# Optimization experiments

Measured on AMD Instinct MI355X. Metric: run time of the kernel, lower is better.

Reference implementation:

```python
import jax, jax.numpy as jnp
import numpy as np

LEAKY_SLOPE = 0.2  # PyG GATConv default negative_slope
EPS = 1e-16


def _gat_layer(h_in, src, dst, W, a_src, a_dst, b, concat):
    # h_in: [N, Fin]; src/dst: [Etot] (self-loops included); W: [Fin, H*C]
    N = h_in.shape[0]
    H, C = a_src.shape
    h = (h_in @ W).reshape(N, H, C)                       # [N,H,C]
    al_s = jnp.sum(h * a_src, axis=-1)                    # [N,H]
    al_d = jnp.sum(h * a_dst, axis=-1)                    # [N,H]
    e = jax.nn.leaky_relu(al_s[src] + al_d[dst], LEAKY_SLOPE)  # [E,H]
    emax = jax.ops.segment_max(e, dst, num_segments=N)    # segment softmax over dst
    p = jnp.exp(e - emax[dst])
    denom = jax.ops.segment_sum(p, dst, num_segments=N)
    alpha = p / (denom[dst] + EPS)                        # [E,H]
    out = jax.ops.segment_sum(h[src] * alpha[:, :, None], dst, num_segments=N)  # [N,H,C]
    out = out.reshape(N, H * C) if concat else out.mean(axis=1)
    return out + b


def setup_inputs() -> dict:
    key = jax.random.key(0)
    ks = jax.random.split(key, 16)
    N, E, Fin, Hd, Hh = 10000, 320000, 256, 128, 4

    def glorot(k, shape, fan_in):
        return jax.random.normal(k, shape, dtype=jnp.float32) * (1.0 / np.sqrt(fan_in))

    inp = {
        "x": jax.random.normal(ks[0], (N, Fin), dtype=jnp.float32),
        "edge_index": jax.random.randint(ks[1], (2, E), 0, N, dtype=jnp.int32),
        # conv1: Fin -> Hd x Hh heads, concat
        "W1": glorot(ks[2], (Fin, Hh * Hd), Fin),
        "a1_src": glorot(ks[3], (Hh, Hd), Hd),
        "a1_dst": glorot(ks[4], (Hh, Hd), Hd),
        "b1": jnp.zeros((Hh * Hd,), jnp.float32),
        # conv2: Hh*Hd -> Hd x Hh heads, concat
        "W2": glorot(ks[5], (Hh * Hd, Hh * Hd), Hh * Hd),
        "a2_src": glorot(ks[6], (Hh, Hd), Hd),
        "a2_dst": glorot(ks[7], (Hh, Hd), Hd),
        "b2": jnp.zeros((Hh * Hd,), jnp.float32),
        # conv3: Hh*Hd -> Hd, 1 head, concat=False (mean)
        "W3": glorot(ks[8], (Hh * Hd, Hd), Hh * Hd),
        "a3_src": glorot(ks[9], (1, Hd), Hd),
        "a3_dst": glorot(ks[10], (1, Hd), Hd),
        "b3": jnp.zeros((Hd,), jnp.float32),
        # classifier: Hd -> Hd//2 -> 2
        "Wc1": glorot(ks[11], (Hd, Hd // 2), Hd),
        "bc1": jnp.zeros((Hd // 2,), jnp.float32),
        "Wc2": glorot(ks[12], (Hd // 2, 2), Hd // 2),
        "bc2": jnp.zeros((2,), jnp.float32),
    }
    return inp


def reference(x, edge_index, W1, a1_src, a1_dst, b1, W2, a2_src, a2_dst, b2,
              W3, a3_src, a3_dst, b3, Wc1, bc1, Wc2, bc2):
    N = x.shape[0]
    loops = jnp.arange(N, dtype=edge_index.dtype)
    src = jnp.concatenate([edge_index[0], loops])  # PyG adds self-loops
    dst = jnp.concatenate([edge_index[1], loops])

    h = jax.nn.elu(_gat_layer(x, src, dst, W1, a1_src, a1_dst, b1, concat=True))
    h = jax.nn.elu(_gat_layer(h, src, dst, W2, a2_src, a2_dst, b2, concat=True))
    embeddings = _gat_layer(h, src, dst, W3, a3_src, a3_dst, b3, concat=False)  # [N, 128]
    out = jax.nn.relu(embeddings @ Wc1 + bc1) @ Wc2 + bc2  # [N, 2]
    return out, embeddings
```

## Files before the change

kernel.cpp:

```cpp
#include <hip/hip_runtime.h>
#include <cstddef>

#define LEAKY 0.2f
#define EPS_DEN 1e-16f

typedef short bf8_t __attribute__((ext_vector_type(8)));
typedef float f4_t __attribute__((ext_vector_type(4)));
typedef unsigned short us4_t __attribute__((ext_vector_type(4)));

__device__ __forceinline__ unsigned short f2bf(float f) {
    unsigned u = __float_as_uint(f);
    unsigned r = (u + 0x7fffu + ((u >> 16) & 1u)) >> 16;
    return (unsigned short)r;
}
__device__ __forceinline__ float bf2f(unsigned short h) {
    return __uint_as_float(((unsigned)h) << 16);
}

__global__ void hist_kernel(const int* __restrict__ dst, int* __restrict__ counts, int E) {
    int i = blockIdx.x * blockDim.x + threadIdx.x;
    if (i < E) atomicAdd(&counts[dst[i]], 1);
}

__global__ void scan1_kernel(int* __restrict__ cnt, int* __restrict__ bsum, int N) {
    __shared__ int s[256];
    int t = threadIdx.x;
    int i = blockIdx.x * 256 + t;
    int v = (i < N) ? cnt[i] : 0;
    s[t] = v;
    __syncthreads();
#pragma unroll
    for (int st = 1; st < 256; st <<= 1) {
        int add = (t >= st) ? s[t - st] : 0;
        __syncthreads();
        s[t] += add;
        __syncthreads();
    }
    if (i < N) cnt[i] = s[t] - v;
    if (t == 255) bsum[blockIdx.x] = s[255];
}

__global__ void scan2_kernel(int* __restrict__ bsum, int* __restrict__ offs, int NB, int N) {
    int t = threadIdx.x;
    int v = (t < NB) ? bsum[t] : 0;
    int inc = v;
#pragma unroll
    for (int off = 1; off < 64; off <<= 1) {
        int u = __shfl_up(inc, off);
        if (t >= off) inc += u;
    }
    if (t < NB) bsum[t] = inc - v;
    if (t == 63) offs[N] = inc;
}

__global__ void scan3_kernel(int* __restrict__ cnt, const int* __restrict__ bsum,
                             int* __restrict__ offs, int N) {
    int i = blockIdx.x * 256 + threadIdx.x;
    if (i < N) {
        int o = cnt[i] + bsum[blockIdx.x];
        offs[i] = o;
        cnt[i] = o;
    }
}

__global__ void scatter_kernel(const int* __restrict__ src, const int* __restrict__ dst,
                               int* __restrict__ cursor, int* __restrict__ csrc, int E) {
    int i = blockIdx.x * blockDim.x + threadIdx.x;
    if (i < E) {
        int d = dst[i];
        int pos = atomicAdd(&cursor[d], 1);
        csrc[pos] = src[i];
    }
}

__global__ void split_kernel(const float* __restrict__ in, unsigned short* __restrict__ hi,
                             unsigned short* __restrict__ lo, int len) {
    int i = blockIdx.x * blockDim.x + threadIdx.x;
    if (i >= len) return;
    float v = in[i];
    unsigned short h = f2bf(v);
    hi[i] = h;
    lo[i] = f2bf(v - bf2f(h));
}

__global__ void wsplit_kernel(const float* __restrict__ W, unsigned short* __restrict__ hi,
                              unsigned short* __restrict__ lo, int K, int N) {
    int idx = blockIdx.x * blockDim.x + threadIdx.x;
    if (idx >= K * N) return;
    int n = idx / K, k = idx % K;
    float v = W[(size_t)k * N + n];
    unsigned short h = f2bf(v);
    hi[idx] = h;
    lo[idx] = f2bf(v - bf2f(h));
}

__global__ __launch_bounds__(256) void mfma_gemm128_kernel(
    const unsigned short* __restrict__ Ahi, const unsigned short* __restrict__ Alo,
    const unsigned short* __restrict__ BThi, const unsigned short* __restrict__ BTlo,
    float* __restrict__ C, int M, int N, int K) {
    constexpr int BK = 32;
    __shared__ __align__(16) unsigned short sA[128 * BK];
    __shared__ __align__(16) unsigned short sB[128 * BK];
    int t = threadIdx.x;
    int w = t >> 6, lane = t & 63;
    int quad = lane >> 4, low = lane & 15;
    int m0 = blockIdx.y * 128, n0 = blockIdx.x * 128;
    int wm = (w & 1) * 64, wn = (w >> 1) * 64;

    f4_t acc[4][4];
#pragma unroll
    for (int i = 0; i < 4; i++)
#pragma unroll
        for (int j = 0; j < 4; j++) acc[i][j] = (f4_t){0.f, 0.f, 0.f, 0.f};

    int srow = lane >> 2;
    int schunk = lane & 3;

    const unsigned short* Ap[3] = {Ahi, Ahi, Alo};
    const unsigned short* Bp[3] = {BThi, BTlo, BThi};

    for (int pass = 0; pass < 3; pass++) {
        const unsigned short* A = Ap[pass];
        const unsigned short* B = Bp[pass];
        for (int k0 = 0; k0 < K; k0 += BK) {
            __syncthreads();
#pragma unroll
            for (int inst = 0; inst < 2; inst++) {
                int r = w * 32 + inst * 16 + srow;
                int gm = m0 + r;
                if (gm >= M) gm = M - 1;
                const void* g = (const void*)(A + (size_t)gm * K + k0 + schunk * 8);
                void* l = (void*)((char*)sA + (size_t)(w * 2048 + inst * 1024));
                __builtin_amdgcn_global_load_lds((const __attribute__((address_space(1))) void*)g,
                                                 (__attribute__((address_space(3))) void*)l, 16, 0, 0);
            }
#pragma unroll
            for (int inst = 0; inst < 2; inst++) {
                int r = w * 32 + inst * 16 + srow;
                int gn = n0 + r;
                const void* g = (const void*)(B + (size_t)gn * K + k0 + schunk * 8);
                void* l = (void*)((char*)sB + (size_t)(w * 2048 + inst * 1024));
                __builtin_amdgcn_global_load_lds((const __attribute__((address_space(1))) void*)g,
                                                 (__attribute__((address_space(3))) void*)l, 16, 0, 0);
            }
            __syncthreads();

            bf8_t af[4], bf[4];
#pragma unroll
            for (int i = 0; i < 4; i++) {
                int row = wm + i * 16 + low;
                af[i] = *(const bf8_t*)&sA[row * BK + quad * 8];
            }
#pragma unroll
            for (int j = 0; j < 4; j++) {
                int row = wn + j * 16 + low;
                bf[j] = *(const bf8_t*)&sB[row * BK + quad * 8];
            }
#pragma unroll
            for (int i = 0; i < 4; i++)
#pragma unroll
                for (int j = 0; j < 4; j++)
                    acc[i][j] = __builtin_amdgcn_mfma_f32_16x16x32_bf16(af[i], bf[j], acc[i][j], 0, 0, 0);
        }
    }

#pragma unroll
    for (int i = 0; i < 4; i++) {
#pragma unroll
        for (int r = 0; r < 4; r++) {
            int gm = m0 + wm + i * 16 + quad * 4 + r;
            if (gm >= M) continue;
#pragma unroll
            for (int j = 0; j < 4; j++) {
                int gn = n0 + wn + j * 16 + low;
                C[(size_t)gm * N + gn] = acc[i][j][r];
            }
        }
    }
}

__global__ __launch_bounds__(256) void mfma_gemm64_kernel(
    const unsigned short* __restrict__ Ahi, const unsigned short* __restrict__ Alo,
    const unsigned short* __restrict__ BThi, const unsigned short* __restrict__ BTlo,
    float* __restrict__ C, int M, int N, int K) {
    constexpr int BK = 32;
    __shared__ __align__(16) unsigned short sA[64 * BK];
    __shared__ __align__(16) unsigned short sB[128 * BK];
    int t = threadIdx.x;
    int w = t >> 6, lane = t & 63;
    int quad = lane >> 4, low = lane & 15;
    int m0 = blockIdx.y * 64, n0 = blockIdx.x * 128;
    int wm = (w & 1) * 32, wn = (w >> 1) * 64;

    f4_t acc[2][4];
#pragma unroll
    for (int i = 0; i < 2; i++)
#pragma unroll
        for (int j = 0; j < 4; j++) acc[i][j] = (f4_t){0.f, 0.f, 0.f, 0.f};

    int srow = lane >> 2;
    int schunk = lane & 3;

    const unsigned short* Ap[3] = {Ahi, Ahi, Alo};
    const unsigned short* Bp[3] = {BThi, BTlo, BThi};

    for (int pass = 0; pass < 3; pass++) {
        const unsigned short* A = Ap[pass];
        const unsigned short* B = Bp[pass];
        for (int k0 = 0; k0 < K; k0 += BK) {
            __syncthreads();
            {
                int gm = m0 + w * 16 + srow;
                if (gm >= M) gm = M - 1;
                const void* g = (const void*)(A + (size_t)gm * K + k0 + schunk * 8);
                void* l = (void*)((char*)sA + (size_t)(w * 1024));
                __builtin_amdgcn_global_load_lds((const __attribute__((address_space(1))) void*)g,
                                                 (__attribute__((address_space(3))) void*)l, 16, 0, 0);
            }
#pragma unroll
            for (int inst = 0; inst < 2; inst++) {
                int gn = n0 + w * 32 + inst * 16 + srow;
                const void* g = (const void*)(B + (size_t)gn * K + k0 + schunk * 8);
                void* l = (void*)((char*)sB + (size_t)(w * 2048 + inst * 1024));
                __builtin_amdgcn_global_load_lds((const __attribute__((address_space(1))) void*)g,
                                                 (__attribute__((address_space(3))) void*)l, 16, 0, 0);
            }
            __syncthreads();

            bf8_t af[2], bf[4];
#pragma unroll
            for (int i = 0; i < 2; i++) {
                int row = wm + i * 16 + low;
                af[i] = *(const bf8_t*)&sA[row * BK + quad * 8];
            }
#pragma unroll
            for (int j = 0; j < 4; j++) {
                int row = wn + j * 16 + low;
                bf[j] = *(const bf8_t*)&sB[row * BK + quad * 8];
            }
#pragma unroll
            for (int i = 0; i < 2; i++)
#pragma unroll
                for (int j = 0; j < 4; j++)
                    acc[i][j] = __builtin_amdgcn_mfma_f32_16x16x32_bf16(af[i], bf[j], acc[i][j], 0, 0, 0);
        }
    }

#pragma unroll
    for (int i = 0; i < 2; i++) {
#pragma unroll
        for (int r = 0; r < 4; r++) {
            int gm = m0 + wm + i * 16 + quad * 4 + r;
            if (gm >= M) continue;
#pragma unroll
            for (int j = 0; j < 4; j++) {
                int gn = n0 + wn + j * 16 + low;
                C[(size_t)gm * N + gn] = acc[i][j][r];
            }
        }
    }
}

__global__ void al_h4_kernel(const float* __restrict__ h, const float* __restrict__ a_src,
                             const float* __restrict__ a_dst, float* __restrict__ als,
                             float* __restrict__ ald, int N) {
    int wave = threadIdx.x >> 6, lane = threadIdx.x & 63;
    int n = blockIdx.x * 4 + wave;
    if (n >= N) return;
    const float* row = h + (size_t)n * 512;
    float ps[4] = {0, 0, 0, 0}, pd[4] = {0, 0, 0, 0};
#pragma unroll
    for (int k = 0; k < 8; k++) {
        int f = k * 64 + lane;
        float v = row[f];
        ps[k >> 1] += v * a_src[f];
        pd[k >> 1] += v * a_dst[f];
    }
#pragma unroll
    for (int off = 32; off; off >>= 1) {
#pragma unroll
        for (int hd = 0; hd < 4; hd++) {
            ps[hd] += __shfl_down(ps[hd], off);
            pd[hd] += __shfl_down(pd[hd], off);
        }
    }
    if (lane == 0) {
#pragma unroll
        for (int hd = 0; hd < 4; hd++) {
            als[n * 4 + hd] = ps[hd];
            ald[n * 4 + hd] = pd[hd];
        }
    }
}

__global__ void al_h1_kernel(const float* __restrict__ h, const float* __restrict__ a_src,
                             const float* __restrict__ a_dst, float* __restrict__ als,
                             float* __restrict__ ald, int N) {
    int wave = threadIdx.x >> 6, lane = threadIdx.x & 63;
    int n = blockIdx.x * 4 + wave;
    if (n >= N) return;
    const float* row = h + (size_t)n * 128;
    float v0 = row[lane], v1 = row[lane + 64];
    float ps = v0 * a_src[lane] + v1 * a_src[lane + 64];
    float pd = v0 * a_dst[lane] + v1 * a_dst[lane + 64];
#pragma unroll
    for (int off = 32; off; off >>= 1) {
        ps += __shfl_down(ps, off);
        pd += __shfl_down(pd, off);
    }
    if (lane == 0) { als[n] = ps; ald[n] = pd; }
}

__global__ void stats_h4_kernel(const int* __restrict__ csrc, const int* __restrict__ offs,
                                const float* __restrict__ als, const float* __restrict__ ald,
                                float* __restrict__ pbuf, float* __restrict__ psf,
                                float* __restrict__ rden, int N, int E) {
    int wave = threadIdx.x >> 6, lane = threadIdx.x & 63;
    int n = blockIdx.x * 4 + wave;
    if (n >= N) return;
    int hd = lane & 3, es = lane >> 2;
    float aldn = ald[n * 4 + hd];
    float selfe = als[n * 4 + hd] + aldn;
    selfe = selfe > 0.f ? selfe : LEAKY * selfe;
    int beg = offs[n], end = offs[n + 1];
    float* pb = pbuf + (size_t)hd * E;
    float m = selfe;
    for (int base = beg; base + es < end; base += 16) {
        int idx = base + es;
        int s = csrc[idx];
        float e = als[s * 4 + hd] + aldn;
        e = e > 0.f ? e : LEAKY * e;
        pb[idx] = e;
        m = fmaxf(m, e);
    }
#pragma unroll
    for (int off = 4; off < 64; off <<= 1) m = fmaxf(m, __shfl_xor(m, off));
    float d = 0.f;
    for (int base = beg; base + es < end; base += 16) {
        int idx = base + es;
        float p = __expf(pb[idx] - m);
        pb[idx] = p;
        d += p;
    }
#pragma unroll
    for (int off = 4; off < 64; off <<= 1) d += __shfl_xor(d, off);
    float pself = __expf(selfe - m);
    float r = 1.0f / (d + pself + EPS_DEN);
    if (es == 0) {
        psf[n * 4 + hd] = pself;
        rden[n * 4 + hd] = r;
    }
}

__global__ void stats_h1_kernel(const int* __restrict__ csrc, const int* __restrict__ offs,
                                const float* __restrict__ als, const float* __restrict__ ald,
                                float* __restrict__ pbuf, float* __restrict__ psf,
                                float* __restrict__ rden, int N) {
    int wave = threadIdx.x >> 6, lane = threadIdx.x & 63;
    int n = blockIdx.x * 4 + wave;
    if (n >= N) return;
    float aldn = ald[n];
    float selfe = als[n] + aldn;
    selfe = selfe > 0.f ? selfe : LEAKY * selfe;
    int beg = offs[n], end = offs[n + 1];
    float m = selfe;
    for (int base = beg; base + lane < end; base += 64) {
        int idx = base + lane;
        int s = csrc[idx];
        float e = als[s] + aldn;
        e = e > 0.f ? e : LEAKY * e;
        pbuf[idx] = e;
        m = fmaxf(m, e);
    }
#pragma unroll
    for (int off = 1; off < 64; off <<= 1) m = fmaxf(m, __shfl_xor(m, off));
    float d = 0.f;
    for (int base = beg; base + lane < end; base += 64) {
        int idx = base + lane;
        float p = __expf(pbuf[idx] - m);
        pbuf[idx] = p;
        d += p;
    }
#pragma unroll
    for (int off = 1; off < 64; off <<= 1) d += __shfl_xor(d, off);
    float pself = __expf(selfe - m);
    float r = 1.0f / (d + pself + EPS_DEN);
    if (lane == 0) { psf[n] = pself; rden[n] = r; }
}

template <bool DO_ELU>
__global__ __launch_bounds__(64) void gat_agg_hh_kernel(
    const float* __restrict__ h, const float* __restrict__ pbuf,
    const float* __restrict__ psf, const float* __restrict__ rden,
    const int* __restrict__ csrc, const int* __restrict__ offs,
    const float* __restrict__ bias, unsigned short* __restrict__ ohi,
    unsigned short* __restrict__ olo, int N, int E) {
    int gid = blockIdx.x;
    int hh = gid & 7;
    int n = gid >> 3;
    int head = hh >> 1;
    int lane = threadIdx.x;
    int eg = lane >> 4;
    int f0 = hh * 64 + (lane & 15) * 4;
    const float* pb = pbuf + (size_t)head * E;

    f4_t acc = (f4_t){0.f, 0.f, 0.f, 0.f};
    __shared__ int sSrc[64];
    __shared__ float sP[64];
    int beg = offs[n], end = offs[n + 1];
    for (int base = beg; base < end; base += 64) {
        int len = min(64, end - base);
        __syncthreads();
        if (lane < len) {
            sSrc[lane] = csrc[base + lane];
            sP[lane] = pb[base + lane];
        }
        __syncthreads();
#pragma unroll 8
        for (int c = eg; c < len; c += 4) {
            const float* srow = h + (size_t)sSrc[c] * 512;
            f4_t x = *(const f4_t*)(srow + f0);
            acc += sP[c] * x;
        }
    }
    if (eg == 0) {
        f4_t x = *(const f4_t*)(h + (size_t)n * 512 + f0);
        acc += psf[n * 4 + head] * x;
    }
#pragma unroll
    for (int j = 0; j < 4; j++) {
        acc[j] += __shfl_xor(acc[j], 16);
        acc[j] += __shfl_xor(acc[j], 32);
    }
    if (lane < 16) {
        float r = rden[n * 4 + head];
        f4_t b = *(const f4_t*)(bias + f0);
        us4_t hs, ls;
#pragma unroll
        for (int j = 0; j < 4; j++) {
            float o = acc[j] * r + b[j];
            if (DO_ELU) o = o > 0.f ? o : (__expf(o) - 1.0f);
            unsigned short hhh = f2bf(o);
            hs[j] = hhh;
            ls[j] = f2bf(o - bf2f(hhh));
        }
        size_t idx = (size_t)n * 512 + f0;
        *(us4_t*)&ohi[idx] = hs;
        *(us4_t*)&olo[idx] = ls;
    }
}

__global__ __launch_bounds__(64) void gat_agg_h1_cls_kernel(
    const float* __restrict__ h, const float* __restrict__ pbuf,
    const float* __restrict__ psf, const float* __restrict__ rden,
    const int* __restrict__ csrc, const int* __restrict__ offs,
    const float* __restrict__ bias, const float* __restrict__ Wc1,
    const float* __restrict__ bc1, const float* __restrict__ Wc2,
    const float* __restrict__ bc2, float* __restrict__ emb,
    float* __restrict__ outp, int N) {
    int n = blockIdx.x;
    int lane = threadIdx.x;
    int half = lane >> 5;
    int f0 = (lane & 31) * 4;

    f4_t acc = (f4_t){0.f, 0.f, 0.f, 0.f};
    __shared__ int sSrc[64];
    __shared__ float sP[64];
    __shared__ float semb[128];
    int beg = offs[n], end = offs[n + 1];
    for (int base = beg; base < end; base += 64) {
        int len = min(64, end - base);
        __syncthreads();
        if (lane < len) {
            sSrc[lane] = csrc[base + lane];
            sP[lane] = pbuf[base + lane];
        }
        __syncthreads();
#pragma unroll 8
        for (int c = half; c < len; c += 2) {
            const float* srow = h + (size_t)sSrc[c] * 128;
            f4_t x = *(const f4_t*)(srow + f0);
            acc += sP[c] * x;
        }
    }
    if (half == 0) {
        f4_t x = *(const f4_t*)(h + (size_t)n * 128 + f0);
        acc += psf[n] * x;
    }
#pragma unroll
    for (int j = 0; j < 4; j++) acc[j] += __shfl_xor(acc[j], 32);

    __syncthreads();
    if (half == 0) {
        float r = rden[n];
        f4_t b = *(const f4_t*)(bias + f0);
        f4_t o;
#pragma unroll
        for (int j = 0; j < 4; j++) o[j] = acc[j] * r + b[j];
        *(f4_t*)&semb[f0] = o;
        *(f4_t*)&emb[(size_t)n * 128 + f0] = o;
    }
    __syncthreads();

    float cacc = bc1[lane];
#pragma unroll 4
    for (int k = 0; k < 128; k++) cacc += semb[k] * Wc1[k * 64 + lane];
    cacc = fmaxf(cacc, 0.f);
    float o0 = cacc * Wc2[lane * 2 + 0];
    float o1 = cacc * Wc2[lane * 2 + 1];
#pragma unroll
    for (int off = 32; off; off >>= 1) {
        o0 += __shfl_down(o0, off);
        o1 += __shfl_down(o1, off);
    }
    if (lane == 0) {
        outp[n * 2 + 0] = o0 + bc2[0];
        outp[n * 2 + 1] = o1 + bc2[1];
    }
}

extern "C" void kernel_launch(void* const* d_in, const int* in_sizes, int n_in,
                              void* d_out, int out_size, void* d_ws, size_t ws_size,
                              hipStream_t stream) {
    const float* x      = (const float*)d_in[0];
    const int*   ei     = (const int*)d_in[1];
    const float* W1     = (const float*)d_in[2];
    const float* a1s    = (const float*)d_in[3];
    const float* a1d    = (const float*)d_in[4];
    const float* b1     = (const float*)d_in[5];
    const float* W2     = (const float*)d_in[6];
    const float* a2s    = (const float*)d_in[7];
    const float* a2d    = (const float*)d_in[8];
    const float* b2     = (const float*)d_in[9];
    const float* W3     = (const float*)d_in[10];
    const float* a3s    = (const float*)d_in[11];
    const float* a3d    = (const float*)d_in[12];
    const float* b3     = (const float*)d_in[13];
    const float* Wc1    = (const float*)d_in[14];
    const float* bc1    = (const float*)d_in[15];
    const float* Wc2    = (const float*)d_in[16];
    const float* bc2    = (const float*)d_in[17];

    const int N = in_sizes[0] / 256;
    const int E = in_sizes[1] / 2;
    const int F = 512;

    const int* src = ei;
    const int* dst = ei + E;

    auto align = [](size_t o) { return (o + 255) & ~(size_t)255; };
    size_t o = 0;
    size_t o_G     = o; o = align(o + (size_t)N * F * 4);
    size_t o_ahi   = o; o = align(o + (size_t)N * F * 2);
    size_t o_alo   = o; o = align(o + (size_t)N * F * 2);
    size_t o_xhi   = o; o = align(o + (size_t)N * 256 * 2);
    size_t o_xlo   = o; o = align(o + (size_t)N * 256 * 2);
    size_t o_w1h   = o; o = align(o + (size_t)512 * 256 * 2);
    size_t o_w1l   = o; o = align(o + (size_t)512 * 256 * 2);
    size_t o_w2h   = o; o = align(o + (size_t)512 * 512 * 2);
    size_t o_w2l   = o; o = align(o + (size_t)512 * 512 * 2);
    size_t o_w3h   = o; o = align(o + (size_t)128 * 512 * 2);
    size_t o_w3l   = o; o = align(o + (size_t)128 * 512 * 2);
    size_t o_als   = o; o = align(o + (size_t)N * 4 * 4);
    size_t o_ald   = o; o = align(o + (size_t)N * 4 * 4);
    size_t o_psf   = o; o = align(o + (size_t)N * 4 * 4);
    size_t o_rden  = o; o = align(o + (size_t)N * 4 * 4);
    size_t o_cnt   = o; o = align(o + (size_t)N * 4);
    size_t o_off   = o; o = align(o + (size_t)(N + 1) * 4);
    size_t o_bsum  = o; o = align(o + (size_t)64 * 4);
    size_t o_csrc  = o; o = align(o + (size_t)E * 4);
    size_t o_ebuf  = o; o = align(o + (size_t)E * 4 * 4);
    (void)ws_size;

    char* ws = (char*)d_ws;
    float* bufG  = (float*)(ws + o_G);
    unsigned short* act_hi = (unsigned short*)(ws + o_ahi);
    unsigned short* act_lo = (unsigned short*)(ws + o_alo);
    unsigned short* x_hi   = (unsigned short*)(ws + o_xhi);
    unsigned short* x_lo   = (unsigned short*)(ws + o_xlo);
    unsigned short* w1h = (unsigned short*)(ws + o_w1h);
    unsigned short* w1l = (unsigned short*)(ws + o_w1l);
    unsigned short* w2h = (unsigned short*)(ws + o_w2h);
    unsigned short* w2l = (unsigned short*)(ws + o_w2l);
    unsigned short* w3h = (unsigned short*)(ws + o_w3h);
    unsigned short* w3l = (unsigned short*)(ws + o_w3l);
    float* als  = (float*)(ws + o_als);
    float* ald  = (float*)(ws + o_ald);
    float* psf  = (float*)(ws + o_psf);
    float* rden = (float*)(ws + o_rden);
    int*   cnt  = (int*)(ws + o_cnt);
    int*   offs = (int*)(ws + o_off);
    int*   bsum = (int*)(ws + o_bsum);
    int*   csrc = (int*)(ws + o_csrc);
    float* ebuf = (float*)(ws + o_ebuf);

    float* outp = (float*)d_out;
    float* emb  = (float*)d_out + (size_t)N * 2;

    hipMemsetAsync(cnt, 0, (size_t)N * 4, stream);
    int eb = (E + 255) / 256;
    int nbs = (N + 255) / 256;
    hipLaunchKernelGGL(hist_kernel, dim3(eb), dim3(256), 0, stream, dst, cnt, E);
    hipLaunchKernelGGL(scan1_kernel, dim3(nbs), dim3(256), 0, stream, cnt, bsum, N);
    hipLaunchKernelGGL(scan2_kernel, dim3(1), dim3(64), 0, stream, bsum, offs, nbs, N);
    hipLaunchKernelGGL(scan3_kernel, dim3(nbs), dim3(256), 0, stream, cnt, bsum, offs, N);
    hipLaunchKernelGGL(scatter_kernel, dim3(eb), dim3(256), 0, stream, src, dst, cnt, csrc, E);

    hipLaunchKernelGGL(split_kernel, dim3((N * 256 + 255) / 256), dim3(256), 0, stream,
                       x, x_hi, x_lo, N * 256);
    hipLaunchKernelGGL(wsplit_kernel, dim3((256 * 512 + 255) / 256), dim3(256), 0, stream,
                       W1, w1h, w1l, 256, 512);
    hipLaunchKernelGGL(wsplit_kernel, dim3((512 * 512 + 255) / 256), dim3(256), 0, stream,
                       W2, w2h, w2l, 512, 512);
    hipLaunchKernelGGL(wsplit_kernel, dim3((512 * 128 + 255) / 256), dim3(256), 0, stream,
                       W3, w3h, w3l, 512, 128);

    int nb4 = (N + 3) / 4;
    int gy128 = (N + 127) / 128;
    int gy64  = (N + 63) / 64;

    hipLaunchKernelGGL(mfma_gemm128_kernel, dim3(512 / 128, gy128), dim3(256), 0, stream,
                       x_hi, x_lo, w1h, w1l, bufG, N, 512, 256);
    hipLaunchKernelGGL(al_h4_kernel, dim3(nb4), dim3(256), 0, stream, bufG, a1s, a1d, als, ald, N);
    hipLaunchKernelGGL(stats_h4_kernel, dim3(nb4), dim3(256), 0, stream,
                       csrc, offs, als, ald, ebuf, psf, rden, N, E);
    hipLaunchKernelGGL((gat_agg_hh_kernel<true>), dim3(N * 8), dim3(64), 0, stream,
                       bufG, ebuf, psf, rden, csrc, offs, b1, act_hi, act_lo, N, E);

    hipLaunchKernelGGL(mfma_gemm128_kernel, dim3(512 / 128, gy128), dim3(256), 0, stream,
                       act_hi, act_lo, w2h, w2l, bufG, N, 512, 512);
    hipLaunchKernelGGL(al_h4_kernel, dim3(nb4), dim3(256), 0, stream, bufG, a2s, a2d, als, ald, N);
    hipLaunchKernelGGL(stats_h4_kernel, dim3(nb4), dim3(256), 0, stream,
                       csrc, offs, als, ald, ebuf, psf, rden, N, E);
    hipLaunchKernelGGL((gat_agg_hh_kernel<true>), dim3(N * 8), dim3(64), 0, stream,
                       bufG, ebuf, psf, rden, csrc, offs, b2, act_hi, act_lo, N, E);

    hipLaunchKernelGGL(mfma_gemm64_kernel, dim3(128 / 128, gy64), dim3(256), 0, stream,
                       act_hi, act_lo, w3h, w3l, bufG, N, 128, 512);
    hipLaunchKernelGGL(al_h1_kernel, dim3(nb4), dim3(256), 0, stream, bufG, a3s, a3d, als, ald, N);
    hipLaunchKernelGGL(stats_h1_kernel, dim3(nb4), dim3(256), 0, stream,
                       csrc, offs, als, ald, ebuf, psf, rden, N);
    hipLaunchKernelGGL(gat_agg_h1_cls_kernel, dim3(N), dim3(64), 0, stream,
                       bufG, ebuf, psf, rden, csrc, offs, b3, Wc1, bc1, Wc2, bc2, emb, outp, N);
}
```

Measured before the change: 391.7 us.

## Fuse split-bf16 GEMM passes into one K loop and drop LDS staging in aggregation

The two split-precision bf16 MFMA GEMMs used to make three separate passes over K, reloading tiles each time. They now load the hi and lo tiles of A and B together per K step and reuse the hi fragments across all three MFMA products. This cuts global-to-LDS traffic and barrier count, at the cost of double the LDS footprint per block. The aggregation kernels also stop staging edge indices and weights through shared memory with barriers. Each lane now reads its edges directly, covering 8 features with more edge groups in flight.

Result: faster. 383.5 us (-2.1%).

```diff
diff --git a/kernel.cpp b/kernel.cpp
--- a/kernel.cpp
+++ b/kernel.cpp
@@ -7,6 +7,7 @@
 typedef short bf8_t __attribute__((ext_vector_type(8)));
 typedef float f4_t __attribute__((ext_vector_type(4)));
 typedef unsigned short us4_t __attribute__((ext_vector_type(4)));
+typedef unsigned short us8_t __attribute__((ext_vector_type(8)));
 
 __device__ __forceinline__ unsigned short f2bf(float f) {
     unsigned u = __float_as_uint(f);
@@ -99,8 +100,10 @@
     const unsigned short* __restrict__ BThi, const unsigned short* __restrict__ BTlo,
     float* __restrict__ C, int M, int N, int K) {
     constexpr int BK = 32;
-    __shared__ __align__(16) unsigned short sA[128 * BK];
-    __shared__ __align__(16) unsigned short sB[128 * BK];
+    __shared__ __align__(16) unsigned short sAh[128 * BK];
+    __shared__ __align__(16) unsigned short sAl[128 * BK];
+    __shared__ __align__(16) unsigned short sBh[128 * BK];
+    __shared__ __align__(16) unsigned short sBl[128 * BK];
     int t = threadIdx.x;
     int w = t >> 6, lane = t & 63;
     int quad = lane >> 4, low = lane & 15;
@@ -116,52 +119,73 @@
     int srow = lane >> 2;
     int schunk = lane & 3;
 
-    const unsigned short* Ap[3] = {Ahi, Ahi, Alo};
-    const unsigned short* Bp[3] = {BThi, BTlo, BThi};
-
-    for (int pass = 0; pass < 3; pass++) {
-        const unsigned short* A = Ap[pass];
-        const unsigned short* B = Bp[pass];
-        for (int k0 = 0; k0 < K; k0 += BK) {
-            __syncthreads();
-#pragma unroll
-            for (int inst = 0; inst < 2; inst++) {
-                int r = w * 32 + inst * 16 + srow;
-                int gm = m0 + r;
-                if (gm >= M) gm = M - 1;
-                const void* g = (const void*)(A + (size_t)gm * K + k0 + schunk * 8);
-                void* l = (void*)((char*)sA + (size_t)(w * 2048 + inst * 1024));
-                __builtin_amdgcn_global_load_lds((const __attribute__((address_space(1))) void*)g,
-                                                 (__attribute__((address_space(3))) void*)l, 16, 0, 0);
-            }
-#pragma unroll
-            for (int inst = 0; inst < 2; inst++) {
-                int r = w * 32 + inst * 16 + srow;
-                int gn = n0 + r;
-                const void* g = (const void*)(B + (size_t)gn * K + k0 + schunk * 8);
-                void* l = (void*)((char*)sB + (size_t)(w * 2048 + inst * 1024));
-                __builtin_amdgcn_global_load_lds((const __attribute__((address_space(1))) void*)g,
-                                                 (__attribute__((address_space(3))) void*)l, 16, 0, 0);
-            }
-            __syncthreads();
-
-            bf8_t af[4], bf[4];
-#pragma unroll
-            for (int i = 0; i < 4; i++) {
-                int row = wm + i * 16 + low;
-                af[i] = *(const bf8_t*)&sA[row * BK + quad * 8];
-            }
-#pragma unroll
-            for (int j = 0; j < 4; j++) {
-                int row = wn + j * 16 + low;
-                bf[j] = *(const bf8_t*)&sB[row * BK + quad * 8];
-            }
-#pragma unroll
-            for (int i = 0; i < 4; i++)
-#pragma unroll
-                for (int j = 0; j < 4; j++)
-                    acc[i][j] = __builtin_amdgcn_mfma_f32_16x16x32_bf16(af[i], bf[j], acc[i][j], 0, 0, 0);
-        }
+    for (int k0 = 0; k0 < K; k0 += BK) {
+        __syncthreads();
+#pragma unroll
+        for (int inst = 0; inst < 2; inst++) {
+            int r = w * 32 + inst * 16 + srow;
+            int gm = m0 + r;
+            if (gm >= M) gm = M - 1;
+            size_t goff = (size_t)gm * K + k0 + schunk * 8;
+            size_t loff = (size_t)(w * 2048 + inst * 1024);
+            __builtin_amdgcn_global_load_lds(
+                (const __attribute__((address_space(1))) void*)(Ahi + goff),
+                (__attribute__((address_space(3))) void*)((char*)sAh + loff), 16, 0, 0);
+            __builtin_amdgcn_global_load_lds(
+                (const __attribute__((address_space(1))) void*)(Alo + goff),
+                (__attribute__((address_space(3))) void*)((char*)sAl + loff), 16, 0, 0);
+        }
+#pragma unroll
+        for (int inst = 0; inst < 2; inst++) {
+            int r = w * 32 + inst * 16 + srow;
+            int gn = n0 + r;
+            size_t goff = (size_t)gn * K + k0 + schunk * 8;
+            size_t loff = (size_t)(w * 2048 + inst * 1024);
+            __builtin_amdgcn_global_load_lds(
+                (const __attribute__((address_space(1))) void*)(BThi + goff),
+                (__attribute__((address_space(3))) void*)((char*)sBh + loff), 16, 0, 0);
+            __builtin_amdgcn_global_load_lds(
+                (const __attribute__((address_space(1))) void*)(BTlo + goff),
+                (__attribute__((address_space(3))) void*)((char*)sBl + loff), 16, 0, 0);
+        }
+        __syncthreads();
+
+        bf8_t afh[4], bfh[4], x[4];
+#pragma unroll
+        for (int i = 0; i < 4; i++) {
+            int row = wm + i * 16 + low;
+            afh[i] = *(const bf8_t*)&sAh[row * BK + quad * 8];
+        }
+#pragma unroll
+        for (int j = 0; j < 4; j++) {
+            int row = wn + j * 16 + low;
+            bfh[j] = *(const bf8_t*)&sBh[row * BK + quad * 8];
+        }
+#pragma unroll
+        for (int i = 0; i < 4; i++)
+#pragma unroll
+            for (int j = 0; j < 4; j++)
+                acc[i][j] = __builtin_amdgcn_mfma_f32_16x16x32_bf16(afh[i], bfh[j], acc[i][j], 0, 0, 0);
+#pragma unroll
+        for (int j = 0; j < 4; j++) {
+            int row = wn + j * 16 + low;
+            x[j] = *(const bf8_t*)&sBl[row * BK + quad * 8];
+        }
+#pragma unroll
+        for (int i = 0; i < 4; i++)
+#pragma unroll
+            for (int j = 0; j < 4; j++)
+                acc[i][j] = __builtin_amdgcn_mfma_f32_16x16x32_bf16(afh[i], x[j], acc[i][j], 0, 0, 0);
+#pragma unroll
+        for (int i = 0; i < 4; i++) {
+            int row = wm + i * 16 + low;
+            x[i] = *(const bf8_t*)&sAl[row * BK + quad * 8];
+        }
+#pragma unroll
+        for (int i = 0; i < 4; i++)
+#pragma unroll
+            for (int j = 0; j < 4; j++)
+                acc[i][j] = __builtin_amdgcn_mfma_f32_16x16x32_bf16(x[i], bfh[j], acc[i][j], 0, 0, 0);
     }
 
 #pragma unroll
@@ -184,8 +208,10 @@
     const unsigned short* __restrict__ BThi, const unsigned short* __restrict__ BTlo,
     float* __restrict__ C, int M, int N, int K) {
     constexpr int BK = 32;
-    __shared__ __align__(16) unsigned short sA[64 * BK];
-    __shared__ __align__(16) unsigned short sB[128 * BK];
+    __shared__ __align__(16) unsigned short sAh[64 * BK];
+    __shared__ __align__(16) unsigned short sAl[64 * BK];
+    __shared__ __align__(16) unsigned short sBh[128 * BK];
+    __shared__ __align__(16) unsigned short sBl[128 * BK];
     int t = threadIdx.x;
     int w = t >> 6, lane = t & 63;
     int quad = lane >> 4, low = lane & 15;
@@ -201,49 +227,70 @@
     int srow = lane >> 2;
     int schunk = lane & 3;
 
-    const unsigned short* Ap[3] = {Ahi, Ahi, Alo};
-    const unsigned short* Bp[3] = {BThi, BTlo, BThi};
-
-    for (int pass = 0; pass < 3; pass++) {
-        const unsigned short* A = Ap[pass];
-        const unsigned short* B = Bp[pass];
-        for (int k0 = 0; k0 < K; k0 += BK) {
-            __syncthreads();
-            {
-                int gm = m0 + w * 16 + srow;
-                if (gm >= M) gm = M - 1;
-                const void* g = (const void*)(A + (size_t)gm * K + k0 + schunk * 8);
-                void* l = (void*)((char*)sA + (size_t)(w * 1024));
-                __builtin_amdgcn_global_load_lds((const __attribute__((address_space(1))) void*)g,
-                                                 (__attribute__((address_space(3))) void*)l, 16, 0, 0);
-            }
-#pragma unroll
-            for (int inst = 0; inst < 2; inst++) {
-                int gn = n0 + w * 32 + inst * 16 + srow;
-                const void* g = (const void*)(B + (size_t)gn * K + k0 + schunk * 8);
-                void* l = (void*)((char*)sB + (size_t)(w * 2048 + inst * 1024));
-                __builtin_amdgcn_global_load_lds((const __attribute__((address_space(1))) void*)g,
-                                                 (__attribute__((address_space(3))) void*)l, 16, 0, 0);
-            }
-            __syncthreads();
-
-            bf8_t af[2], bf[4];
-#pragma unroll
-            for (int i = 0; i < 2; i++) {
-                int row = wm + i * 16 + low;
-                af[i] = *(const bf8_t*)&sA[row * BK + quad * 8];
-            }
-#pragma unroll
-            for (int j = 0; j < 4; j++) {
-                int row = wn + j * 16 + low;
-                bf[j] = *(const bf8_t*)&sB[row * BK + quad * 8];
-            }
-#pragma unroll
-            for (int i = 0; i < 2; i++)
-#pragma unroll
-                for (int j = 0; j < 4; j++)
-                    acc[i][j] = __builtin_amdgcn_mfma_f32_16x16x32_bf16(af[i], bf[j], acc[i][j], 0, 0, 0);
-        }
+    for (int k0 = 0; k0 < K; k0 += BK) {
+        __syncthreads();
+        {
+            int gm = m0 + w * 16 + srow;
+            if (gm >= M) gm = M - 1;
+            size_t goff = (size_t)gm * K + k0 + schunk * 8;
+            size_t loff = (size_t)(w * 1024);
+            __builtin_amdgcn_global_load_lds(
+                (const __attribute__((address_space(1))) void*)(Ahi + goff),
+                (__attribute__((address_space(3))) void*)((char*)sAh + loff), 16, 0, 0);
+            __builtin_amdgcn_global_load_lds(
+                (const __attribute__((address_space(1))) void*)(Alo + goff),
+                (__attribute__((address_space(3))) void*)((char*)sAl + loff), 16, 0, 0);
+        }
+#pragma unroll
+        for (int inst = 0; inst < 2; inst++) {
+            int gn = n0 + w * 32 + inst * 16 + srow;
+            size_t goff = (size_t)gn * K + k0 + schunk * 8;
+            size_t loff = (size_t)(w * 2048 + inst * 1024);
+            __builtin_amdgcn_global_load_lds(
+                (const __attribute__((address_space(1))) void*)(BThi + goff),
+                (__attribute__((address_space(3))) void*)((char*)sBh + loff), 16, 0, 0);
+            __builtin_amdgcn_global_load_lds(
+                (const __attribute__((address_space(1))) void*)(BTlo + goff),
+                (__attribute__((address_space(3))) void*)((char*)sBl + loff), 16, 0, 0);
+        }
+        __syncthreads();
+
+        bf8_t afh[2], bfh[4], x[4];
+#pragma unroll
+        for (int i = 0; i < 2; i++) {
+            int row = wm + i * 16 + low;
+            afh[i] = *(const bf8_t*)&sAh[row * BK + quad * 8];
+        }
+#pragma unroll
+        for (int j = 0; j < 4; j++) {
+            int row = wn + j * 16 + low;
+            bfh[j] = *(const bf8_t*)&sBh[row * BK + quad * 8];
+        }
+#pragma unroll
+        for (int i = 0; i < 2; i++)
+#pragma unroll
+            for (int j = 0; j < 4; j++)
+                acc[i][j] = __builtin_amdgcn_mfma_f32_16x16x32_bf16(afh[i], bfh[j], acc[i][j], 0, 0, 0);
+#pragma unroll
+        for (int j = 0; j < 4; j++) {
+            int row = wn + j * 16 + low;
+            x[j] = *(const bf8_t*)&sBl[row * BK + quad * 8];
+        }
+#pragma unroll
+        for (int i = 0; i < 2; i++)
+#pragma unroll
+            for (int j = 0; j < 4; j++)
+                acc[i][j] = __builtin_amdgcn_mfma_f32_16x16x32_bf16(afh[i], x[j], acc[i][j], 0, 0, 0);
+#pragma unroll
+        for (int i = 0; i < 2; i++) {
+            int row = wm + i * 16 + low;
+            x[i] = *(const bf8_t*)&sAl[row * BK + quad * 8];
+        }
+#pragma unroll
+        for (int i = 0; i < 2; i++)
+#pragma unroll
+            for (int j = 0; j < 4; j++)
+                acc[i][j] = __builtin_amdgcn_mfma_f32_16x16x32_bf16(x[i], bfh[j], acc[i][j], 0, 0, 0);
     }
 
 #pragma unroll
@@ -400,53 +447,64 @@
     int n = gid >> 3;
     int head = hh >> 1;
     int lane = threadIdx.x;
-    int eg = lane >> 4;
-    int f0 = hh * 64 + (lane & 15) * 4;
+    int eg = lane >> 3;
+    int fl = (lane & 7) * 8;
+    int f0 = hh * 64 + fl;
     const float* pb = pbuf + (size_t)head * E;
-
-    f4_t acc = (f4_t){0.f, 0.f, 0.f, 0.f};
-    __shared__ int sSrc[64];
-    __shared__ float sP[64];
     int beg = offs[n], end = offs[n + 1];
-    for (int base = beg; base < end; base += 64) {
-        int len = min(64, end - base);
-        __syncthreads();
-        if (lane < len) {
-            sSrc[lane] = csrc[base + lane];
-            sP[lane] = pb[base + lane];
-        }
-        __syncthreads();
-#pragma unroll 8
-        for (int c = eg; c < len; c += 4) {
-            const float* srow = h + (size_t)sSrc[c] * 512;
-            f4_t x = *(const f4_t*)(srow + f0);
-            acc += sP[c] * x;
-        }
+
+    f4_t a0 = (f4_t){0.f, 0.f, 0.f, 0.f};
+    f4_t a1 = (f4_t){0.f, 0.f, 0.f, 0.f};
+#pragma unroll 2
+    for (int c = beg + eg; c < end; c += 8) {
+        int s = csrc[c];
+        float p = pb[c];
+        const float* srow = h + (size_t)s * 512 + f0;
+        f4_t x0 = *(const f4_t*)(srow);
+        f4_t x1 = *(const f4_t*)(srow + 4);
+        a0 += p * x0;
+        a1 += p * x1;
     }
     if (eg == 0) {
-        f4_t x = *(const f4_t*)(h + (size_t)n * 512 + f0);
-        acc += psf[n * 4 + head] * x;
+        float p = psf[n * 4 + head];
+        const float* srow = h + (size_t)n * 512 + f0;
+        a0 += p * *(const f4_t*)(srow);
+        a1 += p * *(const f4_t*)(srow + 4);
     }
 #pragma unroll
     for (int j = 0; j < 4; j++) {
-        acc[j] += __shfl_xor(acc[j], 16);
-        acc[j] += __shfl_xor(acc[j], 32);
-    }
-    if (lane < 16) {
+        a0[j] += __shfl_xor(a0[j], 8);
+        a0[j] += __shfl_xor(a0[j], 16);
+        a0[j] += __shfl_xor(a0[j], 32);
+        a1[j] += __shfl_xor(a1[j], 8);
+        a1[j] += __shfl_xor(a1[j], 16);
+        a1[j] += __shfl_xor(a1[j], 32);
+    }
+    if (lane < 8) {
+        int fo = hh * 64 + lane * 8;
         float r = rden[n * 4 + head];
-        f4_t b = *(const f4_t*)(bias + f0);
-        us4_t hs, ls;
+        f4_t b0 = *(const f4_t*)(bias + fo);
+        f4_t b1 = *(const f4_t*)(bias + fo + 4);
+        us8_t hs, ls;
 #pragma unroll
         for (int j = 0; j < 4; j++) {
-            float o = acc[j] * r + b[j];
+            float o = a0[j] * r + b0[j];
             if (DO_ELU) o = o > 0.f ? o : (__expf(o) - 1.0f);
-            unsigned short hhh = f2bf(o);
-            hs[j] = hhh;
-            ls[j] = f2bf(o - bf2f(hhh));
-        }
-        size_t idx = (size_t)n * 512 + f0;
-        *(us4_t*)&ohi[idx] = hs;
-        *(us4_t*)&olo[idx] = ls;
+            unsigned short hv = f2bf(o);
+            hs[j] = hv;
+            ls[j] = f2bf(o - bf2f(hv));
+        }
+#pragma unroll
+        for (int j = 0; j < 4; j++) {
+            float o = a1[j] * r + b1[j];
+            if (DO_ELU) o = o > 0.f ? o : (__expf(o) - 1.0f);
+            unsigned short hv = f2bf(o);
+            hs[4 + j] = hv;
+            ls[4 + j] = f2bf(o - bf2f(hv));
+        }
+        size_t idx = (size_t)n * 512 + fo;
+        *(us8_t*)&ohi[idx] = hs;
+        *(us8_t*)&olo[idx] = ls;
     }
 }
 
@@ -460,45 +518,49 @@
     float* __restrict__ outp, int N) {
     int n = blockIdx.x;
     int lane = threadIdx.x;
-    int half = lane >> 5;
-    int f0 = (lane & 31) * 4;
-
-    f4_t acc = (f4_t){0.f, 0.f, 0.f, 0.f};
-    __shared__ int sSrc[64];
-    __shared__ float sP[64];
+    int eg = lane >> 4;
+    int fl = (lane & 15) * 8;
     __shared__ float semb[128];
     int beg = offs[n], end = offs[n + 1];
-    for (int base = beg; base < end; base += 64) {
-        int len = min(64, end - base);
-        __syncthreads();
-        if (lane < len) {
-            sSrc[lane] = csrc[base + lane];
-            sP[lane] = pbuf[base + lane];
-        }
-        __syncthreads();
-#pragma unroll 8
-        for (int c = half; c < len; c += 2) {
-            const float* srow = h + (size_t)sSrc[c] * 128;
-            f4_t x = *(const f4_t*)(srow + f0);
-            acc += sP[c] * x;
-        }
-    }
-    if (half == 0) {
-        f4_t x = *(const f4_t*)(h + (size_t)n * 128 + f0);
-        acc += psf[n] * x;
-    }
-#pragma unroll
-    for (int j = 0; j < 4; j++) acc[j] += __shfl_xor(acc[j], 32);
-
-    __syncthreads();
-    if (half == 0) {
+
+    f4_t a0 = (f4_t){0.f, 0.f, 0.f, 0.f};
+    f4_t a1 = (f4_t){0.f, 0.f, 0.f, 0.f};
+#pragma unroll 2
+    for (int c = beg + eg; c < end; c += 4) {
+        int s = csrc[c];
+        float p = pbuf[c];
+        const float* srow = h + (size_t)s * 128 + fl;
+        a0 += p * *(const f4_t*)(srow);
+        a1 += p * *(const f4_t*)(srow + 4);
+    }
+    if (eg == 0) {
+        float p = psf[n];
+        const float* srow = h + (size_t)n * 128 + fl;
+        a0 += p * *(const f4_t*)(srow);
+        a1 += p * *(const f4_t*)(srow + 4);
+    }
+#pragma unroll
+    for (int j = 0; j < 4; j++) {
+        a0[j] += __shfl_xor(a0[j], 16);
+        a0[j] += __shfl_xor(a0[j], 32);
+        a1[j] += __shfl_xor(a1[j], 16);
+        a1[j] += __shfl_xor(a1[j], 32);
+    }
+    if (lane < 16) {
+        int fo = lane * 8;
         float r = rden[n];
-        f4_t b = *(const f4_t*)(bias + f0);
-        f4_t o;
-#pragma unroll
-        for (int j = 0; j < 4; j++) o[j] = acc[j] * r + b[j];
-        *(f4_t*)&semb[f0] = o;
-        *(f4_t*)&emb[(size_t)n * 128 + f0] = o;
+        f4_t b0 = *(const f4_t*)(bias + fo);
+        f4_t b1 = *(const f4_t*)(bias + fo + 4);
+        f4_t o0, o1;
+#pragma unroll
+        for (int j = 0; j < 4; j++) {
+            o0[j] = a0[j] * r + b0[j];
+            o1[j] = a1[j] * r + b1[j];
+        }
+        *(f4_t*)&semb[fo] = o0;
+        *(f4_t*)&semb[fo + 4] = o1;
+        *(f4_t*)&emb[(size_t)n * 128 + fo] = o0;
+        *(f4_t*)&emb[(size_t)n * 128 + fo + 4] = o1;
     }
     __syncthreads();
 
```
